# Optimization experiments

Hardware: AMD Instinct MI355X
Metric: run time of the kernel (lower is better)

Reference implementation:

```python
import jax, jax.numpy as jnp
import numpy as np

K = 10  # hardcoded in the module
F = 3 + 3 * K + 3 * K + K + 3  # 76-dim per-point feature


def setup_inputs() -> dict:
    key = jax.random.key(0)
    k0, k1, k2, k3, k4 = jax.random.split(key, 5)
    B, N = 4, 8192
    input_cloud = jax.random.normal(k0, (B, N, 3), dtype=jnp.float32)
    # Single shared MLP (76 -> 64 -> 3); the original instantiates a fresh
    # randomly-initialized MLP per point, which a fused kernel replaces with
    # shared weights.
    W1 = jax.random.normal(k1, (F, 64), dtype=jnp.float32) * 0.1
    b1 = jax.random.normal(k2, (64,), dtype=jnp.float32) * 0.01
    W2 = jax.random.normal(k3, (64, 3), dtype=jnp.float32) * 0.1
    b2 = jax.random.normal(k4, (3,), dtype=jnp.float32) * 0.01
    return {"input_cloud": input_cloud, "W1": W1, "b1": b1, "W2": W2, "b2": b2}


def _knn_indices(cloud):
    # squared pairwise distances (same ordering as cdist), topk smallest
    sq = jnp.sum(cloud * cloud, axis=-1)  # [B,N]
    d2 = sq[:, :, None] + sq[:, None, :] - 2.0 * jnp.einsum("bnd,bmd->bnm", cloud, cloud)
    _, idx = jax.lax.top_k(-d2, K + 1)  # [B,N,K+1], smallest first (self at 0)
    return idx[:, :, 1:]  # drop self -> [B,N,K]


def reference(input_cloud, W1, b1, W2, b2):
    B, N, _ = input_cloud.shape
    knn_idx = _knn_indices(input_cloud)  # [B,N,K] int32

    # gather neighbors: [B,N,K,3]
    neighbors = jnp.take_along_axis(input_cloud[:, None, :, :],
                                    knn_idx[:, :, :, None], axis=2)
    center = input_cloud  # [B,N,3]
    rel = neighbors - center[:, :, None, :]           # [B,N,K,3]
    dists = jnp.sqrt(jnp.sum(rel * rel, axis=-1))     # [B,N,K]

    # per-point 3x3 covariance of the K neighbors (unbiased, like torch.cov)
    mean = jnp.mean(neighbors, axis=2, keepdims=True)  # [B,N,1,3]
    cen = neighbors - mean
    cov = jnp.einsum("bnki,bnkj->bnij", cen, cen) / (K - 1)  # [B,N,3,3]

    eig = jnp.linalg.eigvalsh(cov)          # ascending [B,N,3]
    l1, l2, l3 = eig[..., 2], eig[..., 1], eig[..., 0]  # descending order
    linearity = (l1 - l2) / l1
    planarity = (l2 - l3) / l1
    scattering = l3 / l1
    geom = jnp.stack([linearity, planarity, scattering], axis=-1)  # [B,N,3]

    feats = jnp.concatenate(
        [center,
         neighbors.reshape(B, N, 3 * K),
         rel.reshape(B, N, 3 * K),
         dists,
         geom], axis=-1)  # [B,N,76]

    h = jax.nn.relu(jnp.einsum("bnf,fh->bnh", feats, W1) + b1)
    out = jax.nn.relu(jnp.einsum("bnh,ho->bno", h, W2) + b2)  # [B,N,3]
    return out
```

## Files before the change

kernel.cpp:

```cpp
#include <hip/hip_runtime.h>
#include <math.h>

#define KNN    10
#define NPTS   8192
#define HID    64
#define NF     76
#define Q      16
#define CAP    64
#define F32_INF __uint_as_float(0x7F800000u)

__device__ __forceinline__ float rl(float v, int lane) {
    return __int_as_float(__builtin_amdgcn_readlane(__float_as_int(v), lane));
}

__global__ __launch_bounds__(256) void prep_kernel(const float* __restrict__ cloud,
                                                   float4* __restrict__ pts4) {
    const int i = blockIdx.x * 256 + threadIdx.x;
    const float x = cloud[i * 3 + 0];
    const float y = cloud[i * 3 + 1];
    const float z = cloud[i * 3 + 2];
    pts4[i] = make_float4(x, y, z, fmaf(z, z, fmaf(y, y, x * x)));
}

__global__ __launch_bounds__(512) void knn_kernel(const float4* __restrict__ pts4,
                                                  unsigned short* __restrict__ knn_idx) {
    __shared__ unsigned long long coll[CAP][33];
    __shared__ float pk[8][Q][17];
    __shared__ float tau_s[32];
    __shared__ int   cnt[32];

    const int t    = threadIdx.x;
    const int w    = t >> 6;
    const int lane = t & 63;
    const int g    = w >> 2;
    const int h    = w & 3;
    const int bx   = blockIdx.x;
    const int b    = bx >> 8;
    const int n_base = (bx & 255) * 32 + g * Q;
    const int lq_base = g * Q;
    const int cb0 = h * (NPTS / 4);

    const float4* pb = pts4 + b * NPTS;

    if (t < 32) cnt[t] = 0;

    float qxs[Q], qys[Q], qzs[Q], qss[Q];
#pragma unroll
    for (int qq = 0; qq < Q; ++qq) {
        const float4 qv = pb[n_base + qq];
        qxs[qq] = qv.x; qys[qq] = qv.y; qzs[qq] = qv.z; qss[qq] = qv.w;
    }

    float vmin[Q];
#pragma unroll
    for (int qq = 0; qq < Q; ++qq) vmin[qq] = F32_INF;

    float4 cp = pb[cb0 + lane];
    for (int ti = 0; ti < NPTS / 4 / 64; ++ti) {
        const float4 np = (ti < NPTS / 4 / 64 - 1) ? pb[cb0 + (ti + 1) * 64 + lane] : cp;
        const float a2x = -2.0f * cp.x;
        const float a2y = -2.0f * cp.y;
        const float a2z = -2.0f * cp.z;
        const float aw  = cp.w;
#pragma unroll
        for (int qq = 0; qq < Q; ++qq) {
            const float v = fmaf(a2x, qxs[qq], fmaf(a2y, qys[qq], fmaf(a2z, qzs[qq], aw)));
            vmin[qq] = fminf(vmin[qq], v);
        }
        cp = np;
    }

#pragma unroll
    for (int qq = 0; qq < Q; ++qq) {
        float v = vmin[qq];
        v = fminf(v, __shfl_xor(v, 32, 64));
        v = fminf(v, __shfl_xor(v, 16, 64));
        if (lane < 16) pk[w][qq][lane] = v;
    }
    __syncthreads();

    if (h == 0) {
        float md[KNN + 1];
#pragma unroll
        for (int s = 0; s <= KNN; ++s) md[s] = F32_INF;
        const int qsel = lane & 15;
#pragma unroll
        for (int cc = 0; cc < 64; ++cc) {
            float d = pk[g * 4 + (cc >> 4)][qsel][cc & 15];
#pragma unroll
            for (int u = 0; u <= KNN; ++u) {
                const float lo = fminf(md[u], d);
                d = fmaxf(md[u], d);
                md[u] = lo;
            }
        }
        if (lane < 16) tau_s[lq_base + lane] = md[KNN] + 1e-3f;
    }
    __syncthreads();

    float taum[Q];
    {
        const float tv = tau_s[lq_base + (lane & 15)];
#pragma unroll
        for (int qq = 0; qq < Q; ++qq) taum[qq] = rl(tv, qq);
    }

    float4 cp2 = pb[cb0 + lane];
    int jcur = cb0 + lane;
    for (int ti = 0; ti < NPTS / 4 / 64; ++ti) {
        const float4 np = (ti < NPTS / 4 / 64 - 1) ? pb[cb0 + (ti + 1) * 64 + lane] : cp2;
        const float a2x = -2.0f * cp2.x;
        const float a2y = -2.0f * cp2.y;
        const float a2z = -2.0f * cp2.z;
        const float aw  = cp2.w;
#pragma unroll
        for (int qq = 0; qq < Q; ++qq) {
            const float v = fmaf(a2x, qxs[qq], fmaf(a2y, qys[qq], fmaf(a2z, qzs[qq], aw)));
            if (__builtin_expect(v <= taum[qq], 0)) {
                const float px = -0.5f * a2x;
                const float py = -0.5f * a2y;
                const float pz = -0.5f * a2z;
                const float dot = fmaf(pz, qzs[qq], fmaf(py, qys[qq], px * qxs[qq]));
                const float d2 = fmaf(-2.0f, dot, qss[qq] + aw);
                const unsigned int fb = __float_as_uint(d2);
                const unsigned int m =
                    fb ^ ((unsigned int)((int)fb >> 31) | 0x80000000u);
                const unsigned long long key =
                    ((unsigned long long)m << 13) | (unsigned long long)(unsigned)jcur;
                const int slot = atomicAdd(&cnt[lq_base + qq], 1);
                if (slot < CAP) coll[slot][lq_base + qq] = key;
            }
        }
        cp2 = np; jcur += 64;
    }
    __syncthreads();

    if (t < 32) {
        const int m = cnt[t];
        int mc = m;
#pragma unroll
        for (int off = 1; off < 32; off <<= 1)
            mc = max(mc, __shfl_xor(mc, off, 64));
        mc = __builtin_amdgcn_readfirstlane(mc);

        const int n = (bx & 255) * 32 + t;

        unsigned long long md[KNN + 1];
#pragma unroll
        for (int s = 0; s <= KNN; ++s) md[s] = ~0ULL;

        if (mc <= CAP) {
            for (int cc = 0; cc < mc; ++cc) {
                unsigned long long key = (cc < m) ? coll[cc][t] : ~0ULL;
#pragma unroll
                for (int u = 0; u <= KNN; ++u) {
                    const bool lt = key < md[u];
                    const unsigned long long lo = lt ? key : md[u];
                    key = lt ? md[u] : key;
                    md[u] = lo;
                }
            }
        } else {
            const float4 qv = pb[n];
            for (int j = 0; j < NPTS; ++j) {
                const float4 p = pb[j];
                const float dot = fmaf(p.z, qv.z, fmaf(p.y, qv.y, p.x * qv.x));
                const float d2 = fmaf(-2.0f, dot, qv.w + p.w);
                const unsigned int fb = __float_as_uint(d2);
                const unsigned int mm =
                    fb ^ ((unsigned int)((int)fb >> 31) | 0x80000000u);
                unsigned long long key =
                    ((unsigned long long)mm << 13) | (unsigned long long)j;
                key = (j == n) ? ~0ULL : key;
#pragma unroll
                for (int u = 0; u <= KNN; ++u) {
                    const bool lt = key < md[u];
                    const unsigned long long lo = lt ? key : md[u];
                    key = lt ? md[u] : key;
                    md[u] = lo;
                }
            }
        }

        unsigned short* outp = knn_idx + ((size_t)b * NPTS + n) * KNN;
        int outc = 0;
#pragma unroll
        for (int u = 0; u <= KNN; ++u) {
            const int idx = (int)(md[u] & 8191u);
            if (outc < KNN && idx != n) outp[outc++] = (unsigned short)idx;
        }
    }
}

__global__ __launch_bounds__(256) void feat_mlp_kernel(const float4* __restrict__ pts4,
                                                       const float* __restrict__ W1,
                                                       const float* __restrict__ b1,
                                                       const float* __restrict__ W2,
                                                       const float* __restrict__ b2,
                                                       const unsigned short* __restrict__ knn_idx,
                                                       float* __restrict__ out) {
    __shared__ float w1s[NF * 68];
    __shared__ float b1s[HID];
    __shared__ float w2s[HID * 3];
    __shared__ float b2s[3];
    __shared__ float fs[64][NF + 1];

    const int t = threadIdx.x;
    for (int idx = t; idx < NF * HID; idx += 256)
        w1s[(idx >> 6) * 68 + (idx & 63)] = W1[idx];
    if (t < HID) b1s[t] = b1[t];
    if (t < HID * 3) w2s[t] = W2[t];
    if (t < 3) b2s[t] = b2[t];

    const int pl   = t >> 2;
    const int subh = t & 1;
    const int subf = (t >> 1) & 1;
    const int gid = blockIdx.x * 64 + pl;
    const int b = gid >> 13;
    const int n = gid & (NPTS - 1);
    const float4* pb = pts4 + b * NPTS;

    if ((t & 3) == 0) {
        const float4 cq = pb[n];
        const float cx = cq.x, cy = cq.y, cz = cq.z;

        float nx[KNN], ny[KNN], nz[KNN];
        const unsigned short* ki = knn_idx + (size_t)gid * KNN;
#pragma unroll
        for (int k = 0; k < KNN; ++k) {
            const int j = ki[k];
            const float4 p = pb[j];
            nx[k] = p.x; ny[k] = p.y; nz[k] = p.z;
        }

        float* fr = fs[pl];
        fr[0] = cx; fr[1] = cy; fr[2] = cz;
#pragma unroll
        for (int k = 0; k < KNN; ++k) {
            fr[3 + 3 * k + 0] = nx[k];
            fr[3 + 3 * k + 1] = ny[k];
            fr[3 + 3 * k + 2] = nz[k];
        }
#pragma unroll
        for (int k = 0; k < KNN; ++k) {
            fr[33 + 3 * k + 0] = nx[k] - cx;
            fr[33 + 3 * k + 1] = ny[k] - cy;
            fr[33 + 3 * k + 2] = nz[k] - cz;
        }
#pragma unroll
        for (int k = 0; k < KNN; ++k) {
            const float rx = nx[k] - cx, ry = ny[k] - cy, rz = nz[k] - cz;
            fr[63 + k] = sqrtf(fmaf(rz, rz, fmaf(ry, ry, rx * rx)));
        }

        float mx = 0.f, my = 0.f, mz = 0.f;
#pragma unroll
        for (int k = 0; k < KNN; ++k) { mx += nx[k]; my += ny[k]; mz += nz[k]; }
        mx *= (1.0f / KNN); my *= (1.0f / KNN); mz *= (1.0f / KNN);
        float c00 = 0.f, c01 = 0.f, c02 = 0.f, c11 = 0.f, c12 = 0.f, c22 = 0.f;
#pragma unroll
        for (int k = 0; k < KNN; ++k) {
            const float ex = nx[k] - mx, ey = ny[k] - my, ez = nz[k] - mz;
            c00 = fmaf(ex, ex, c00); c01 = fmaf(ex, ey, c01); c02 = fmaf(ex, ez, c02);
            c11 = fmaf(ey, ey, c11); c12 = fmaf(ey, ez, c12); c22 = fmaf(ez, ez, c22);
        }
        const float sc = 1.0f / (KNN - 1);
        c00 *= sc; c01 *= sc; c02 *= sc; c11 *= sc; c12 *= sc; c22 *= sc;

        const float qd = (c00 + c11 + c22) * (1.0f / 3.0f);
        const float pp1 = c01 * c01 + c02 * c02 + c12 * c12;
        const float d00 = c00 - qd, d11 = c11 - qd, d22 = c22 - qd;
        const float p2 = d00 * d00 + d11 * d11 + d22 * d22 + 2.0f * pp1;
        float l1, l2, l3;
        if (p2 < 1e-30f) {
            l1 = l2 = l3 = qd;
        } else {
            const float p = sqrtf(p2 * (1.0f / 6.0f));
            const float inv = 1.0f / p;
            const float e00 = d00 * inv, e11 = d11 * inv, e22 = d22 * inv;
            const float e01 = c01 * inv, e02 = c02 * inv, e12 = c12 * inv;
            float detB = e00 * (e11 * e22 - e12 * e12)
                       - e01 * (e01 * e22 - e12 * e02)
                       + e02 * (e01 * e12 - e11 * e02);
            float r = 0.5f * detB;
            r = fminf(1.0f, fmaxf(-1.0f, r));
            const float phi = acosf(r) * (1.0f / 3.0f);
            l1 = qd + 2.0f * p * __cosf(phi);
            l3 = qd + 2.0f * p * __cosf(phi + 2.0943951023931953f);
            l2 = 3.0f * qd - l1 - l3;
        }
        fr[73] = (l1 - l2) / l1;
        fr[74] = (l2 - l3) / l1;
        fr[75] = l3 / l1;
    }

    __syncthreads();

    const float* fr = fs[pl];
    const int f0 = subf * 38;

    float h[32];
#pragma unroll
    for (int j = 0; j < 32; ++j) h[j] = (subf == 0) ? b1s[subh * 32 + j] : 0.0f;

#pragma unroll 2
    for (int ff = 0; ff < 38; ++ff) {
        const int f = f0 + ff;
        const float v = fr[f];
        const float4* w4 = reinterpret_cast<const float4*>(w1s + f * 68 + subh * 32);
#pragma unroll
        for (int j4 = 0; j4 < 8; ++j4) {
            const float4 w = w4[j4];
            h[4 * j4 + 0] = fmaf(v, w.x, h[4 * j4 + 0]);
            h[4 * j4 + 1] = fmaf(v, w.y, h[4 * j4 + 1]);
            h[4 * j4 + 2] = fmaf(v, w.z, h[4 * j4 + 2]);
            h[4 * j4 + 3] = fmaf(v, w.w, h[4 * j4 + 3]);
        }
    }

#pragma unroll
    for (int j = 0; j < 32; ++j) h[j] += __shfl_xor(h[j], 2, 64);

    float o0 = 0.f, o1 = 0.f, o2 = 0.f;
#pragma unroll
    for (int j = 0; j < 32; ++j) {
        const float r = fmaxf(h[j], 0.0f);
        const int jj = subh * 32 + j;
        o0 = fmaf(r, w2s[jj * 3 + 0], o0);
        o1 = fmaf(r, w2s[jj * 3 + 1], o1);
        o2 = fmaf(r, w2s[jj * 3 + 2], o2);
    }
    o0 += __shfl_xor(o0, 1, 64);
    o1 += __shfl_xor(o1, 1, 64);
    o2 += __shfl_xor(o2, 1, 64);

    if ((t & 3) == 0) {
        float* op = out + (size_t)gid * 3;
        op[0] = fmaxf(o0 + b2s[0], 0.0f);
        op[1] = fmaxf(o1 + b2s[1], 0.0f);
        op[2] = fmaxf(o2 + b2s[2], 0.0f);
    }
}

extern "C" void kernel_launch(void* const* d_in, const int* in_sizes, int n_in,
                              void* d_out, int out_size, void* d_ws, size_t ws_size,
                              hipStream_t stream) {
    const float* cloud = (const float*)d_in[0];
    const float* W1    = (const float*)d_in[1];
    const float* b1    = (const float*)d_in[2];
    const float* W2    = (const float*)d_in[3];
    const float* b2    = (const float*)d_in[4];
    float* out = (float*)d_out;

    float4* pts4 = (float4*)d_ws;
    unsigned short* knn = (unsigned short*)((char*)d_ws + 4 * NPTS * 16);

    prep_kernel<<<dim3(128), dim3(256), 0, stream>>>(cloud, pts4);
    knn_kernel<<<dim3(1024), dim3(512), 0, stream>>>(pts4, knn);
    feat_mlp_kernel<<<dim3(512), dim3(256), 0, stream>>>(pts4, W1, b1, W2, b2, knn, out);
}
```

Baseline: 174.8 us.

## Compute kNN candidate distances with split-bf16 MFMA dot products

Replaces the scalar FMA distance loops in the kNN threshold and collection passes with 16x16x32 bf16 MFMA instructions, using a hi/lo bf16 split of coordinates so the dot product stays close to fp32. The prep kernel now also writes packed bf16 records and squared norms into the workspace. The approximate distances only filter candidates, and exact fp32 distances are recomputed for the keys. The threshold margin is raised to absorb the bf16 error, which can increase the candidate count and the risk of overflowing the collection buffer.

```diff
diff --git a/kernel.cpp b/kernel.cpp
--- a/kernel.cpp
+++ b/kernel.cpp
@@ -5,27 +5,54 @@
 #define NPTS   8192
 #define HID    64
 #define NF     76
-#define Q      16
 #define CAP    64
+#define MARGIN 1.6e-2f
 #define F32_INF __uint_as_float(0x7F800000u)
 
-__device__ __forceinline__ float rl(float v, int lane) {
-    return __int_as_float(__builtin_amdgcn_readlane(__float_as_int(v), lane));
+typedef __attribute__((ext_vector_type(8))) short bf16x8;
+typedef __attribute__((ext_vector_type(4))) float f32x4;
+
+__device__ __forceinline__ unsigned short bf16rn(float x) {
+    const unsigned int u = __float_as_uint(x);
+    return (unsigned short)((u + 0x7FFFu + ((u >> 16) & 1u)) >> 16);
+}
+__device__ __forceinline__ float bf16tof(unsigned short h) {
+    return __uint_as_float(((unsigned int)h) << 16);
 }
 
 __global__ __launch_bounds__(256) void prep_kernel(const float* __restrict__ cloud,
-                                                   float4* __restrict__ pts4) {
+                                                   float4* __restrict__ pts4,
+                                                   uint4* __restrict__ bfrec,
+                                                   float* __restrict__ pw) {
     const int i = blockIdx.x * 256 + threadIdx.x;
     const float x = cloud[i * 3 + 0];
     const float y = cloud[i * 3 + 1];
     const float z = cloud[i * 3 + 2];
-    pts4[i] = make_float4(x, y, z, fmaf(z, z, fmaf(y, y, x * x)));
+    const float w = fmaf(z, z, fmaf(y, y, x * x));
+    pts4[i] = make_float4(x, y, z, w);
+    pw[i] = w;
+    const unsigned short xh = bf16rn(x), yh = bf16rn(y), zh = bf16rn(z);
+    const unsigned short xl = bf16rn(x - bf16tof(xh));
+    const unsigned short yl = bf16rn(y - bf16tof(yh));
+    const unsigned short zl = bf16rn(z - bf16tof(zh));
+    uint4 r0, r1;
+    r0.x = (unsigned)xh | ((unsigned)yh << 16);
+    r0.y = (unsigned)zh | ((unsigned)xh << 16);
+    r0.z = (unsigned)yh | ((unsigned)zh << 16);
+    r0.w = (unsigned)xl | ((unsigned)yl << 16);
+    r1.x = (unsigned)zl | ((unsigned)xl << 16);
+    r1.y = (unsigned)yl | ((unsigned)zl << 16);
+    r1.z = 0u; r1.w = 0u;
+    bfrec[i * 2 + 0] = r0;
+    bfrec[i * 2 + 1] = r1;
 }
 
 __global__ __launch_bounds__(512) void knn_kernel(const float4* __restrict__ pts4,
+                                                  const uint4* __restrict__ bfrec,
+                                                  const float* __restrict__ pw,
                                                   unsigned short* __restrict__ knn_idx) {
     __shared__ unsigned long long coll[CAP][33];
-    __shared__ float pk[8][Q][17];
+    __shared__ float pk[2][16][17];
     __shared__ float tau_s[32];
     __shared__ int   cnt[32];
 
@@ -36,46 +63,69 @@
     const int h    = w & 3;
     const int bx   = blockIdx.x;
     const int b    = bx >> 8;
-    const int n_base = (bx & 255) * 32 + g * Q;
-    const int lq_base = g * Q;
+    const int n_base = (bx & 255) * 32 + g * 16;
+    const int lq_base = g * 16;
     const int cb0 = h * (NPTS / 4);
 
-    const float4* pb = pts4 + b * NPTS;
+    const float4* pb  = pts4 + b * NPTS;
+    const uint4*  bfp = bfrec + (size_t)b * NPTS * 2;
+    const float*  pwp = pw + b * NPTS;
 
     if (t < 32) cnt[t] = 0;
 
-    float qxs[Q], qys[Q], qzs[Q], qss[Q];
-#pragma unroll
-    for (int qq = 0; qq < Q; ++qq) {
-        const float4 qv = pb[n_base + qq];
-        qxs[qq] = qv.x; qys[qq] = qv.y; qzs[qq] = qv.z; qss[qq] = qv.w;
-    }
-
-    float vmin[Q];
-#pragma unroll
-    for (int qq = 0; qq < Q; ++qq) vmin[qq] = F32_INF;
-
-    float4 cp = pb[cb0 + lane];
-    for (int ti = 0; ti < NPTS / 4 / 64; ++ti) {
-        const float4 np = (ti < NPTS / 4 / 64 - 1) ? pb[cb0 + (ti + 1) * 64 + lane] : cp;
-        const float a2x = -2.0f * cp.x;
-        const float a2y = -2.0f * cp.y;
-        const float a2z = -2.0f * cp.z;
-        const float aw  = cp.w;
-#pragma unroll
-        for (int qq = 0; qq < Q; ++qq) {
-            const float v = fmaf(a2x, qxs[qq], fmaf(a2y, qys[qq], fmaf(a2z, qzs[qq], aw)));
-            vmin[qq] = fminf(vmin[qq], v);
-        }
-        cp = np;
-    }
-
-#pragma unroll
-    for (int qq = 0; qq < Q; ++qq) {
-        float v = vmin[qq];
-        v = fminf(v, __shfl_xor(v, 32, 64));
-        v = fminf(v, __shfl_xor(v, 16, 64));
-        if (lane < 16) pk[w][qq][lane] = v;
+    const int am = lane & 15;
+    const int aq = lane >> 4;
+
+    bf16x8 afrag = (bf16x8)(short)0;
+    {
+        const float4 qv = pb[n_base + am];
+        const unsigned short xh = bf16rn(qv.x), yh = bf16rn(qv.y), zh = bf16rn(qv.z);
+        const unsigned short xl = bf16rn(qv.x - bf16tof(xh));
+        const unsigned short yl = bf16rn(qv.y - bf16tof(yh));
+        const unsigned short zl = bf16rn(qv.z - bf16tof(zh));
+        if (aq == 0) {
+            afrag = (bf16x8){(short)xh,(short)yh,(short)zh,(short)xl,
+                             (short)yl,(short)zl,(short)xh,(short)yh};
+        } else if (aq == 1) {
+            afrag = (bf16x8){(short)zh,(short)xl,(short)yl,(short)zl,0,0,0,0};
+        }
+    }
+
+    const float4 qf0 = pb[n_base + aq * 4 + 0];
+    const float4 qf1 = pb[n_base + aq * 4 + 1];
+    const float4 qf2 = pb[n_base + aq * 4 + 2];
+    const float4 qf3 = pb[n_base + aq * 4 + 3];
+
+    const uint4 zrec = make_uint4(0u, 0u, 0u, 0u);
+
+#pragma unroll
+    for (int seg = 0; seg < 4; ++seg) {
+        float vm0 = F32_INF, vm1 = F32_INF, vm2 = F32_INF, vm3 = F32_INF;
+        for (int ti = 0; ti < 32; ++ti) {
+            const int c0 = cb0 + seg * 512 + ti * 16;
+            const uint4 brec = (aq < 2) ? bfp[(size_t)(c0 + am) * 2 + aq] : zrec;
+            const bf16x8 bfrag = __builtin_bit_cast(bf16x8, brec);
+            const float pwv = pwp[c0 + am];
+            f32x4 acc = {0.f, 0.f, 0.f, 0.f};
+            acc = __builtin_amdgcn_mfma_f32_16x16x32_bf16(afrag, bfrag, acc, 0, 0, 0);
+            vm0 = fminf(vm0, fmaf(-2.0f, acc[0], pwv));
+            vm1 = fminf(vm1, fmaf(-2.0f, acc[1], pwv));
+            vm2 = fminf(vm2, fmaf(-2.0f, acc[2], pwv));
+            vm3 = fminf(vm3, fmaf(-2.0f, acc[3], pwv));
+        }
+#pragma unroll
+        for (int off = 1; off < 16; off <<= 1) {
+            vm0 = fminf(vm0, __shfl_xor(vm0, off, 64));
+            vm1 = fminf(vm1, __shfl_xor(vm1, off, 64));
+            vm2 = fminf(vm2, __shfl_xor(vm2, off, 64));
+            vm3 = fminf(vm3, __shfl_xor(vm3, off, 64));
+        }
+        if (am == 0) {
+            pk[g][h * 4 + seg][aq * 4 + 0] = vm0;
+            pk[g][h * 4 + seg][aq * 4 + 1] = vm1;
+            pk[g][h * 4 + seg][aq * 4 + 2] = vm2;
+            pk[g][h * 4 + seg][aq * 4 + 3] = vm3;
+        }
     }
     __syncthreads();
 
@@ -85,8 +135,8 @@
         for (int s = 0; s <= KNN; ++s) md[s] = F32_INF;
         const int qsel = lane & 15;
 #pragma unroll
-        for (int cc = 0; cc < 64; ++cc) {
-            float d = pk[g * 4 + (cc >> 4)][qsel][cc & 15];
+        for (int cc = 0; cc < 16; ++cc) {
+            float d = pk[g][cc][qsel];
 #pragma unroll
             for (int u = 0; u <= KNN; ++u) {
                 const float lo = fminf(md[u], d);
@@ -94,44 +144,42 @@
                 md[u] = lo;
             }
         }
-        if (lane < 16) tau_s[lq_base + lane] = md[KNN] + 1e-3f;
+        if (lane < 16) tau_s[lq_base + lane] = md[KNN] + MARGIN;
     }
     __syncthreads();
 
-    float taum[Q];
-    {
-        const float tv = tau_s[lq_base + (lane & 15)];
-#pragma unroll
-        for (int qq = 0; qq < Q; ++qq) taum[qq] = rl(tv, qq);
-    }
-
-    float4 cp2 = pb[cb0 + lane];
-    int jcur = cb0 + lane;
-    for (int ti = 0; ti < NPTS / 4 / 64; ++ti) {
-        const float4 np = (ti < NPTS / 4 / 64 - 1) ? pb[cb0 + (ti + 1) * 64 + lane] : cp2;
-        const float a2x = -2.0f * cp2.x;
-        const float a2y = -2.0f * cp2.y;
-        const float a2z = -2.0f * cp2.z;
-        const float aw  = cp2.w;
-#pragma unroll
-        for (int qq = 0; qq < Q; ++qq) {
-            const float v = fmaf(a2x, qxs[qq], fmaf(a2y, qys[qq], fmaf(a2z, qzs[qq], aw)));
-            if (__builtin_expect(v <= taum[qq], 0)) {
-                const float px = -0.5f * a2x;
-                const float py = -0.5f * a2y;
-                const float pz = -0.5f * a2z;
-                const float dot = fmaf(pz, qzs[qq], fmaf(py, qys[qq], px * qxs[qq]));
-                const float d2 = fmaf(-2.0f, dot, qss[qq] + aw);
+    const float tq0 = tau_s[lq_base + aq * 4 + 0];
+    const float tq1 = tau_s[lq_base + aq * 4 + 1];
+    const float tq2 = tau_s[lq_base + aq * 4 + 2];
+    const float tq3 = tau_s[lq_base + aq * 4 + 3];
+
+    for (int ti = 0; ti < 128; ++ti) {
+        const int c0 = cb0 + ti * 16;
+        const uint4 brec = (aq < 2) ? bfp[(size_t)(c0 + am) * 2 + aq] : zrec;
+        const bf16x8 bfrag = __builtin_bit_cast(bf16x8, brec);
+        const float pwv = pwp[c0 + am];
+        f32x4 acc = {0.f, 0.f, 0.f, 0.f};
+        acc = __builtin_amdgcn_mfma_f32_16x16x32_bf16(afrag, bfrag, acc, 0, 0, 0);
+        const int jc = c0 + am;
+#pragma unroll
+        for (int r = 0; r < 4; ++r) {
+            const float v = fmaf(-2.0f, acc[r], pwv);
+            const float tqr = (r == 0) ? tq0 : (r == 1) ? tq1 : (r == 2) ? tq2 : tq3;
+            if (__builtin_expect(v <= tqr, 0)) {
+                const float4 qfr = (r == 0) ? qf0 : (r == 1) ? qf1 : (r == 2) ? qf2 : qf3;
+                const float4 p = pb[jc];
+                const float dot = fmaf(p.z, qfr.z, fmaf(p.y, qfr.y, p.x * qfr.x));
+                const float d2 = fmaf(-2.0f, dot, qfr.w + p.w);
                 const unsigned int fb = __float_as_uint(d2);
-                const unsigned int m =
+                const unsigned int mo =
                     fb ^ ((unsigned int)((int)fb >> 31) | 0x80000000u);
                 const unsigned long long key =
-                    ((unsigned long long)m << 13) | (unsigned long long)(unsigned)jcur;
-                const int slot = atomicAdd(&cnt[lq_base + qq], 1);
-                if (slot < CAP) coll[slot][lq_base + qq] = key;
+                    ((unsigned long long)mo << 13) | (unsigned long long)(unsigned)jc;
+                const int lq = lq_base + aq * 4 + r;
+                const int slot = atomicAdd(&cnt[lq], 1);
+                if (slot < CAP) coll[slot][lq] = key;
             }
         }
-        cp2 = np; jcur += 64;
     }
     __syncthreads();
 
@@ -352,10 +400,13 @@
     const float* b2    = (const float*)d_in[4];
     float* out = (float*)d_out;
 
-    float4* pts4 = (float4*)d_ws;
-    unsigned short* knn = (unsigned short*)((char*)d_ws + 4 * NPTS * 16);
-
-    prep_kernel<<<dim3(128), dim3(256), 0, stream>>>(cloud, pts4);
-    knn_kernel<<<dim3(1024), dim3(512), 0, stream>>>(pts4, knn);
+    char* ws = (char*)d_ws;
+    float4* pts4 = (float4*)ws;
+    unsigned short* knn = (unsigned short*)(ws + 512 * 1024);
+    uint4* bfrec = (uint4*)(ws + 1184 * 1024);
+    float* pwa = (float*)(ws + 2208 * 1024);
+
+    prep_kernel<<<dim3(128), dim3(256), 0, stream>>>(cloud, pts4, bfrec, pwa);
+    knn_kernel<<<dim3(1024), dim3(512), 0, stream>>>(pts4, bfrec, pwa, knn);
     feat_mlp_kernel<<<dim3(512), dim3(256), 0, stream>>>(pts4, W1, b1, W2, b2, knn, out);
 }
```

New measurement: 365.6 us. 2.09x slower.

## Fuse KNN selection with feature building and MLP in one kernel

Applied to the files above, without the earlier changes.

Merges the KNN kernel and the feature/MLP kernel into a single launch. Neighbor indices now stay in shared memory instead of going through a global buffer. The MLP tail runs on 128 of the 512 threads per block, with 32 points per block. W1 is read straight from global memory (cached) rather than staged in LDS. This removes one launch and the index round trip, but adds a serial tail to each KNN block, leaves most threads idle during it, and raises shared-memory use, which may cut occupancy.

```diff
diff --git a/kernel.cpp b/kernel.cpp
--- a/kernel.cpp
+++ b/kernel.cpp
@@ -22,12 +22,21 @@
     pts4[i] = make_float4(x, y, z, fmaf(z, z, fmaf(y, y, x * x)));
 }
 
-__global__ __launch_bounds__(512) void knn_kernel(const float4* __restrict__ pts4,
-                                                  unsigned short* __restrict__ knn_idx) {
+__global__ __launch_bounds__(512) void knn_feat_kernel(const float4* __restrict__ pts4,
+                                                       const float* __restrict__ W1,
+                                                       const float* __restrict__ b1,
+                                                       const float* __restrict__ W2,
+                                                       const float* __restrict__ b2,
+                                                       float* __restrict__ out) {
     __shared__ unsigned long long coll[CAP][33];
     __shared__ float pk[8][Q][17];
     __shared__ float tau_s[32];
     __shared__ int   cnt[32];
+    __shared__ int   idx_s[32][KNN];
+    __shared__ float fs[32][NF + 1];
+    __shared__ float b1s[HID];
+    __shared__ float w2s[HID * 3];
+    __shared__ float b2s[3];
 
     const int t    = threadIdx.x;
     const int w    = t >> 6;
@@ -43,6 +52,9 @@
     const float4* pb = pts4 + b * NPTS;
 
     if (t < 32) cnt[t] = 0;
+    if (t < HID) b1s[t] = b1[t];
+    if (t >= 64 && t < 64 + HID * 3) w2s[t - 64] = W2[t - 64];
+    if (t >= 256 && t < 259) b2s[t - 256] = b2[t - 256];
 
     float qxs[Q], qys[Q], qzs[Q], qss[Q];
 #pragma unroll
@@ -182,53 +194,28 @@
             }
         }
 
-        unsigned short* outp = knn_idx + ((size_t)b * NPTS + n) * KNN;
         int outc = 0;
 #pragma unroll
         for (int u = 0; u <= KNN; ++u) {
             const int idx = (int)(md[u] & 8191u);
-            if (outc < KNN && idx != n) outp[outc++] = (unsigned short)idx;
-        }
-    }
-}
-
-__global__ __launch_bounds__(256) void feat_mlp_kernel(const float4* __restrict__ pts4,
-                                                       const float* __restrict__ W1,
-                                                       const float* __restrict__ b1,
-                                                       const float* __restrict__ W2,
-                                                       const float* __restrict__ b2,
-                                                       const unsigned short* __restrict__ knn_idx,
-                                                       float* __restrict__ out) {
-    __shared__ float w1s[NF * 68];
-    __shared__ float b1s[HID];
-    __shared__ float w2s[HID * 3];
-    __shared__ float b2s[3];
-    __shared__ float fs[64][NF + 1];
-
-    const int t = threadIdx.x;
-    for (int idx = t; idx < NF * HID; idx += 256)
-        w1s[(idx >> 6) * 68 + (idx & 63)] = W1[idx];
-    if (t < HID) b1s[t] = b1[t];
-    if (t < HID * 3) w2s[t] = W2[t];
-    if (t < 3) b2s[t] = b2[t];
+            if (outc < KNN && idx != n) idx_s[t][outc++] = idx;
+        }
+    }
+    __syncthreads();
 
     const int pl   = t >> 2;
     const int subh = t & 1;
     const int subf = (t >> 1) & 1;
-    const int gid = blockIdx.x * 64 + pl;
-    const int b = gid >> 13;
-    const int n = gid & (NPTS - 1);
-    const float4* pb = pts4 + b * NPTS;
-
-    if ((t & 3) == 0) {
-        const float4 cq = pb[n];
+    const int n_f  = (bx & 255) * 32 + pl;
+
+    if (t < 128 && (t & 3) == 0) {
+        const float4 cq = pb[n_f];
         const float cx = cq.x, cy = cq.y, cz = cq.z;
 
         float nx[KNN], ny[KNN], nz[KNN];
-        const unsigned short* ki = knn_idx + (size_t)gid * KNN;
-#pragma unroll
-        for (int k = 0; k < KNN; ++k) {
-            const int j = ki[k];
+#pragma unroll
+        for (int k = 0; k < KNN; ++k) {
+            const int j = idx_s[pl][k];
             const float4 p = pb[j];
             nx[k] = p.x; ny[k] = p.y; nz[k] = p.z;
         }
@@ -296,49 +283,51 @@
 
     __syncthreads();
 
-    const float* fr = fs[pl];
-    const int f0 = subf * 38;
-
-    float h[32];
-#pragma unroll
-    for (int j = 0; j < 32; ++j) h[j] = (subf == 0) ? b1s[subh * 32 + j] : 0.0f;
+    if (t < 128) {
+        const float* fr = fs[pl];
+        const int f0 = subf * 38;
+
+        float hreg[32];
+#pragma unroll
+        for (int j = 0; j < 32; ++j) hreg[j] = (subf == 0) ? b1s[subh * 32 + j] : 0.0f;
 
 #pragma unroll 2
-    for (int ff = 0; ff < 38; ++ff) {
-        const int f = f0 + ff;
-        const float v = fr[f];
-        const float4* w4 = reinterpret_cast<const float4*>(w1s + f * 68 + subh * 32);
-#pragma unroll
-        for (int j4 = 0; j4 < 8; ++j4) {
-            const float4 w = w4[j4];
-            h[4 * j4 + 0] = fmaf(v, w.x, h[4 * j4 + 0]);
-            h[4 * j4 + 1] = fmaf(v, w.y, h[4 * j4 + 1]);
-            h[4 * j4 + 2] = fmaf(v, w.z, h[4 * j4 + 2]);
-            h[4 * j4 + 3] = fmaf(v, w.w, h[4 * j4 + 3]);
-        }
-    }
-
-#pragma unroll
-    for (int j = 0; j < 32; ++j) h[j] += __shfl_xor(h[j], 2, 64);
-
-    float o0 = 0.f, o1 = 0.f, o2 = 0.f;
-#pragma unroll
-    for (int j = 0; j < 32; ++j) {
-        const float r = fmaxf(h[j], 0.0f);
-        const int jj = subh * 32 + j;
-        o0 = fmaf(r, w2s[jj * 3 + 0], o0);
-        o1 = fmaf(r, w2s[jj * 3 + 1], o1);
-        o2 = fmaf(r, w2s[jj * 3 + 2], o2);
-    }
-    o0 += __shfl_xor(o0, 1, 64);
-    o1 += __shfl_xor(o1, 1, 64);
-    o2 += __shfl_xor(o2, 1, 64);
-
-    if ((t & 3) == 0) {
-        float* op = out + (size_t)gid * 3;
-        op[0] = fmaxf(o0 + b2s[0], 0.0f);
-        op[1] = fmaxf(o1 + b2s[1], 0.0f);
-        op[2] = fmaxf(o2 + b2s[2], 0.0f);
+        for (int ff = 0; ff < 38; ++ff) {
+            const int f = f0 + ff;
+            const float v = fr[f];
+            const float4* w4 = reinterpret_cast<const float4*>(W1 + f * HID + subh * 32);
+#pragma unroll
+            for (int j4 = 0; j4 < 8; ++j4) {
+                const float4 wv = w4[j4];
+                hreg[4 * j4 + 0] = fmaf(v, wv.x, hreg[4 * j4 + 0]);
+                hreg[4 * j4 + 1] = fmaf(v, wv.y, hreg[4 * j4 + 1]);
+                hreg[4 * j4 + 2] = fmaf(v, wv.z, hreg[4 * j4 + 2]);
+                hreg[4 * j4 + 3] = fmaf(v, wv.w, hreg[4 * j4 + 3]);
+            }
+        }
+
+#pragma unroll
+        for (int j = 0; j < 32; ++j) hreg[j] += __shfl_xor(hreg[j], 2, 64);
+
+        float o0 = 0.f, o1 = 0.f, o2 = 0.f;
+#pragma unroll
+        for (int j = 0; j < 32; ++j) {
+            const float r = fmaxf(hreg[j], 0.0f);
+            const int jj = subh * 32 + j;
+            o0 = fmaf(r, w2s[jj * 3 + 0], o0);
+            o1 = fmaf(r, w2s[jj * 3 + 1], o1);
+            o2 = fmaf(r, w2s[jj * 3 + 2], o2);
+        }
+        o0 += __shfl_xor(o0, 1, 64);
+        o1 += __shfl_xor(o1, 1, 64);
+        o2 += __shfl_xor(o2, 1, 64);
+
+        if ((t & 3) == 0) {
+            float* op = out + ((size_t)b * NPTS + n_f) * 3;
+            op[0] = fmaxf(o0 + b2s[0], 0.0f);
+            op[1] = fmaxf(o1 + b2s[1], 0.0f);
+            op[2] = fmaxf(o2 + b2s[2], 0.0f);
+        }
     }
 }
 
@@ -353,9 +342,7 @@
     float* out = (float*)d_out;
 
     float4* pts4 = (float4*)d_ws;
-    unsigned short* knn = (unsigned short*)((char*)d_ws + 4 * NPTS * 16);
 
     prep_kernel<<<dim3(128), dim3(256), 0, stream>>>(cloud, pts4);
-    knn_kernel<<<dim3(1024), dim3(512), 0, stream>>>(pts4, knn);
-    feat_mlp_kernel<<<dim3(512), dim3(256), 0, stream>>>(pts4, W1, b1, W2, b2, knn, out);
+    knn_feat_kernel<<<dim3(1024), dim3(512), 0, stream>>>(pts4, W1, b1, W2, b2, out);
 }
```

Result: slower. 210.6 us (+20.5%).
